# Optimization experiments

Hardware: AMD Instinct MI355X
Metric: run time of the kernel (lower is better)

The kernel has to match this reference:

```python
import jax, jax.numpy as jnp
import numpy as np

U_NUM, I_NUM, ENV_NUM, FACTOR, NNZ, BATCH = 200000, 100000, 4, 64, 9600000, 16384
N_NODES = U_NUM + I_NUM
N_LAYERS = 2


def setup_inputs() -> dict:
    key = jax.random.key(0)
    ks = jax.random.split(key, 14)
    std = 0.01
    user_inv = jax.random.normal(ks[0], (U_NUM, FACTOR), jnp.float32) * std
    item_inv = jax.random.normal(ks[1], (I_NUM, FACTOR), jnp.float32) * std
    user_env = jax.random.normal(ks[2], (U_NUM, FACTOR), jnp.float32) * std
    item_env = jax.random.normal(ks[3], (I_NUM, FACTOR), jnp.float32) * std
    env_emb = jax.random.normal(ks[4], (ENV_NUM, FACTOR), jnp.float32) * std
    # xavier_uniform for classifier weight [env_num, factor]
    limit = float(np.sqrt(6.0 / (FACTOR + ENV_NUM)))
    clf_W = jax.random.uniform(ks[5], (ENV_NUM, FACTOR), jnp.float32, -limit, limit)
    clf_b = jnp.zeros((ENV_NUM,), jnp.float32)
    rows = jax.random.randint(ks[6], (NNZ,), 0, N_NODES, jnp.int32)
    cols = jax.random.randint(ks[7], (NNZ,), 0, N_NODES, jnp.int32)
    # mimic symmetric-normalized adjacency values ~ 1/deg
    vals = jax.random.uniform(ks[8], (NNZ,), jnp.float32) * (1.0 / 32.0)
    users_id = jax.random.randint(ks[9], (BATCH,), 0, U_NUM, jnp.int64)
    items_id = jax.random.randint(ks[10], (BATCH,), 0, I_NUM, jnp.int64)
    envs_id = jax.random.randint(ks[11], (BATCH,), 0, ENV_NUM, jnp.int64)
    return dict(users_id=users_id, items_id=items_id, envs_id=envs_id,
                alpha=jnp.float32(1.0), rows=rows, cols=cols, vals=vals,
                user_inv=user_inv, item_inv=item_inv, user_env=user_env,
                item_env=item_env, env_emb=env_emb, clf_W=clf_W, clf_b=clf_b)


def _lgn_propagate(u_emb, i_emb, rows, cols, vals):
    # LightGCN: mean of [e, Ae, A^2 e]; SpMM via gather + segment_sum
    cur = jnp.concatenate([u_emb, i_emb], axis=0)  # [N, F]
    acc = cur
    for _ in range(N_LAYERS):
        cur = jax.ops.segment_sum(vals[:, None] * cur[cols], rows,
                                  num_segments=N_NODES)
        acc = acc + cur
    light = acc / float(N_LAYERS + 1)
    return light[:U_NUM], light[U_NUM:]


def reference(users_id, items_id, envs_id, alpha, rows, cols, vals,
              user_inv, item_inv, user_env, item_env, env_emb, clf_W, clf_b):
    u_inv_all, i_inv_all = _lgn_propagate(user_inv, item_inv, rows, cols, vals)
    u_env_all, i_env_all = _lgn_propagate(user_env, item_env, rows, cols, vals)
    ue_inv = u_inv_all[users_id]      # [B, F]
    ie_inv = i_inv_all[items_id]
    ue_env = u_env_all[users_id]
    ie_env = i_env_all[items_id]
    e_emb = env_emb[envs_id]
    inv_pref = ue_inv * ie_inv                       # [B, F]
    env_pref = ue_env * ie_env * e_emb               # [B, F]
    invariant_score = jax.nn.sigmoid(jnp.sum(inv_pref, axis=1))
    env_mid = jax.nn.sigmoid(jnp.sum(env_pref, axis=1))
    env_aware_score = invariant_score * env_mid
    # ReverseLayerF is identity in forward
    logits = inv_pref @ clf_W.T + clf_b              # [B, E]
    env_outputs = jax.nn.log_softmax(logits, axis=1)
    return (invariant_score.reshape(-1), env_aware_score.reshape(-1),
            env_outputs.reshape(-1, ENV_NUM))
```

## Files before the change

kernel.cpp:

```cpp
#include <hip/hip_runtime.h>
#include <hip/hip_bf16.h>

#define FACTOR   64
#define F2       128
#define EMAX     8

#define CRPB     512
#define SH1      9
#define MAXNB1   1024
#define CH       16384
#define HCH      32768
#define CAP      18176

#define QSCALE     256.0f
#define INV_QSCALE 0.00390625f

typedef __hip_bfloat162 bf162;
typedef float        f32x2 __attribute__((ext_vector_type(2)));
typedef unsigned int u32x2 __attribute__((ext_vector_type(2)));
typedef unsigned int u32x4 __attribute__((ext_vector_type(4)));

#if __has_builtin(__builtin_amdgcn_cvt_pk_f32_fp8) && __has_builtin(__builtin_amdgcn_cvt_pk_fp8_f32)
#define HAVE_HW_FP8 1
#endif

__device__ __forceinline__ float fp8_dec_sw(unsigned b) {
    unsigned s = (b & 0x80u) << 24;
    unsigned e = (b >> 3) & 0xF;
    unsigned m = b & 7u;
    if (e == 0) {
        float r = (float)m * 0.001953125f;
        return (b & 0x80u) ? -r : r;
    }
    return __uint_as_float(s | ((e + 120u) << 23) | (m << 20));
}

__device__ __forceinline__ unsigned fp8_enc_sw(float f) {
    unsigned x = __float_as_uint(f);
    unsigned s = (x >> 24) & 0x80u;
    float a = fabsf(f);
    if (a < 0.0009765625f) return s;
    if (a >= 448.f) return s | 0x7Eu;
    int e = (int)((__float_as_uint(a) >> 23)) - 127;
    if (e < -6) {
        int m = (int)(a * 512.f + 0.5f);
        if (m >= 8) return s | 0x08u;
        return s | (unsigned)m;
    }
    unsigned mant = (__float_as_uint(a) >> 20) & 0x7u;
    unsigned rnd  = (__float_as_uint(a) >> 19) & 0x1u;
    unsigned code = ((unsigned)(e + 7) << 3) | mant;
    code += rnd;
    if (code >= 0x7Fu) code = 0x7Eu;
    return s | code;
}

__device__ __forceinline__ float2 fp8x2_lo(unsigned u) {
#ifdef HAVE_HW_FP8
    f32x2 r = __builtin_amdgcn_cvt_pk_f32_fp8((int)u, false);
    float2 o; o.x = r.x; o.y = r.y; return o;
#else
    float2 o; o.x = fp8_dec_sw(u & 0xFFu); o.y = fp8_dec_sw((u >> 8) & 0xFFu); return o;
#endif
}
__device__ __forceinline__ float2 fp8x2_hi(unsigned u) {
#ifdef HAVE_HW_FP8
    f32x2 r = __builtin_amdgcn_cvt_pk_f32_fp8((int)u, true);
    float2 o; o.x = r.x; o.y = r.y; return o;
#else
    float2 o; o.x = fp8_dec_sw((u >> 16) & 0xFFu); o.y = fp8_dec_sw((u >> 24) & 0xFFu); return o;
#endif
}

__device__ __forceinline__ unsigned short f32x2_to_fp8(float a, float b) {
#ifdef HAVE_HW_FP8
    int r = __builtin_amdgcn_cvt_pk_fp8_f32(a, b, 0, false);
    return (unsigned short)(r & 0xFFFF);
#else
    return (unsigned short)(fp8_enc_sw(a) | (fp8_enc_sw(b) << 8));
#endif
}

struct alignas(8) EdgeT { int c; float v; };

__device__ __forceinline__ float wsum(float x) {
#pragma unroll
    for (int o = 32; o > 0; o >>= 1) x += __shfl_xor(x, o, 64);
    return x;
}

__global__ void init_ptr_kernel(int* __restrict__ p, int M) {
    int t = blockIdx.x * blockDim.x + threadIdx.x;
    if (t < M) p[t] = 0;
}

__global__ void bucket_hist_kernel(const int* __restrict__ rows, int* __restrict__ bcnt,
                                   long nnz, int NB1) {
    __shared__ int lc[MAXNB1];
    for (int i = threadIdx.x; i < NB1; i += blockDim.x) lc[i] = 0;
    __syncthreads();
    long base = (long)blockIdx.x * HCH;
    long end  = base + HCH; if (end > nnz) end = nnz;
    if (end - base == HCH) {
        const u32x4* rp = (const u32x4*)(rows + base);
        for (int i = threadIdx.x; i < HCH / 4; i += blockDim.x) {
            u32x4 r4 = __builtin_nontemporal_load(rp + i);
            atomicAdd(&lc[r4.x >> SH1], 1);
            atomicAdd(&lc[r4.y >> SH1], 1);
            atomicAdd(&lc[r4.z >> SH1], 1);
            atomicAdd(&lc[r4.w >> SH1], 1);
        }
    } else {
        for (long e = base + threadIdx.x; e < end; e += blockDim.x)
            atomicAdd(&lc[((unsigned)rows[e]) >> SH1], 1);
    }
    __syncthreads();
    for (int i = threadIdx.x; i < NB1; i += blockDim.x)
        if (lc[i]) atomicAdd(&bcnt[i], lc[i]);
}

__global__ void bucket_scan_kernel(const int* __restrict__ bcnt, int* __restrict__ boff,
                                   int* __restrict__ cursor, int NB1) {
    __shared__ int wsums[4];
    int tid = threadIdx.x;
    int lane = tid & 63, wv = tid >> 6;
    int carry = 0;
    for (int base = 0; base < NB1; base += 1024) {
        int idx = base + tid * 4;
        int v0 = (idx + 0 < NB1) ? bcnt[idx + 0] : 0;
        int v1 = (idx + 1 < NB1) ? bcnt[idx + 1] : 0;
        int v2 = (idx + 2 < NB1) ? bcnt[idx + 2] : 0;
        int v3 = (idx + 3 < NB1) ? bcnt[idx + 3] : 0;
        int s1 = v0 + v1 + v2 + v3;
        int s = s1;
#pragma unroll
        for (int o = 1; o < 64; o <<= 1) { int t = __shfl_up(s, o, 64); if (lane >= o) s += t; }
        if (lane == 63) wsums[wv] = s;
        __syncthreads();
        int woff = 0, total = 0;
#pragma unroll
        for (int i = 0; i < 4; i++) { int t = wsums[i]; if (i < wv) woff += t; total += t; }
        int run = carry + woff + (s - s1);
        if (idx + 0 < NB1) { boff[idx + 0] = run; cursor[idx + 0] = run; } run += v0;
        if (idx + 1 < NB1) { boff[idx + 1] = run; cursor[idx + 1] = run; } run += v1;
        if (idx + 2 < NB1) { boff[idx + 2] = run; cursor[idx + 2] = run; } run += v2;
        if (idx + 3 < NB1) { boff[idx + 3] = run; cursor[idx + 3] = run; } run += v3;
        carry += total;
        __syncthreads();
    }
    if (tid == 0) boff[NB1] = carry;
}

__global__ void partition_kernel(const int* __restrict__ rows, const int* __restrict__ cols,
                                 const float* __restrict__ vals, int* __restrict__ cursor,
                                 EdgeT* __restrict__ staged, long nnz, int NB1) {
    extern __shared__ EdgeT ebuf[];
    __shared__ int lc[MAXNB1];
    __shared__ int lof[MAXNB1];
    __shared__ int lb[MAXNB1];
    __shared__ int wsums[16];
    int tid = threadIdx.x;
    long base = (long)blockIdx.x * CH;
    long end  = base + CH; if (end > nnz) end = nnz;
    int m = (int)(end - base);
    for (int i = tid; i < NB1; i += blockDim.x) lc[i] = 0;
    __syncthreads();
    if (m == CH) {
        const u32x4* rp = (const u32x4*)(rows + base);
        for (int i = tid; i < CH / 4; i += blockDim.x) {
            u32x4 r4 = rp[i];
            atomicAdd(&lc[r4.x >> SH1], 1);
            atomicAdd(&lc[r4.y >> SH1], 1);
            atomicAdd(&lc[r4.z >> SH1], 1);
            atomicAdd(&lc[r4.w >> SH1], 1);
        }
    } else {
        for (int i = tid; i < m; i += blockDim.x)
            atomicAdd(&lc[((unsigned)rows[base + i]) >> SH1], 1);
    }
    __syncthreads();
    int v = (tid < NB1) ? lc[tid] : 0;
    int s = v;
#pragma unroll
    for (int o = 1; o < 64; o <<= 1) { int t = __shfl_up(s, o, 64); if ((tid & 63) >= o) s += t; }
    if ((tid & 63) == 63) wsums[tid >> 6] = s;
    __syncthreads();
    int woff = 0;
#pragma unroll
    for (int i = 0; i < 16; i++) if (i < (tid >> 6)) woff += wsums[i];
    if (tid < NB1) {
        lof[tid] = woff + s - v;
        lb[tid]  = v ? atomicAdd(&cursor[tid], v) : 0;
        lc[tid]  = 0;
    }
    __syncthreads();
    for (int i = tid; i < m; i += blockDim.x) {
        int r = rows[base + i];
        unsigned b = ((unsigned)r) >> SH1;
        int rank = atomicAdd(&lc[b], 1);
        EdgeT E;
        E.c = (int)((((unsigned)r & (CRPB - 1)) << 19) |
                    (unsigned)__builtin_nontemporal_load(cols + base + i));
        E.v = __builtin_nontemporal_load(vals + base + i);
        ebuf[lof[b] + rank] = E;
    }
    __syncthreads();
    int wv = tid >> 6, lane = tid & 63, nwv = blockDim.x >> 6;
    for (int b = wv; b < NB1; b += nwv) {
        int c  = lc[b];
        int lo = lof[b];
        int gb = lb[b];
        for (int j = lane; j < c; j += 64)
            staged[(long)gb + j] = ebuf[lo + j];
    }
}

__global__ void coarse_sort_kernel(const int* __restrict__ boff, const EdgeT* __restrict__ staged,
                                   EdgeT* __restrict__ edges, int* __restrict__ p,
                                   int NB1, int N) {
    extern __shared__ EdgeT le[];
    __shared__ int cnt[CRPB];
    __shared__ int rs[CRPB];
    __shared__ int wsum8[CRPB / 64];
    int b = blockIdx.x;
    int start = boff[b], end = boff[b + 1];
    int m = end - start;
    int tid = threadIdx.x;
    if (tid < CRPB) cnt[tid] = 0;
    __syncthreads();
    for (int i = tid; i < m; i += blockDim.x)
        atomicAdd(&cnt[((unsigned)staged[start + i].c) >> 19], 1);
    __syncthreads();
    int v = (tid < CRPB) ? cnt[tid] : 0;
    int s = v;
#pragma unroll
    for (int o = 1; o < 64; o <<= 1) { int t = __shfl_up(s, o, 64); if ((tid & 63) >= o) s += t; }
    if (tid < CRPB && (tid & 63) == 63) wsum8[tid >> 6] = s;
    __syncthreads();
    if (tid < CRPB) {
        int woff = 0;
        int w = tid >> 6;
#pragma unroll
        for (int i = 0; i < CRPB / 64; i++) if (i < w) woff += wsum8[i];
        int ex = woff + s - v;
        rs[tid] = ex;
        int idx = b * CRPB + tid;
        if (idx <= N) p[idx] = start + ex;
        cnt[tid] = 0;
    }
    if (b == NB1 - 1 && tid == 0) p[N] = end;
    __syncthreads();
    bool fits = (m <= CAP);
    for (int i = tid; i < m; i += blockDim.x) {
        EdgeT E = staged[start + i];
        unsigned key = (unsigned)E.c;
        int rl = key >> 19;
        int rank = atomicAdd(&cnt[rl], 1);
        int pos = rs[rl] + rank;
        EdgeT O; O.c = (int)(key & 0x7FFFFu); O.v = E.v;
        if (fits) le[pos] = O;
        else edges[start + pos] = O;
    }
    __syncthreads();
    if (fits) {
        for (int i = tid; i < m; i += blockDim.x)
            edges[start + i] = le[i];
    }
}

__global__ void pack_x0q_kernel(const float* __restrict__ ui, const float* __restrict__ ii,
                                const float* __restrict__ ue, const float* __restrict__ ie,
                                unsigned short* __restrict__ x0q, int N, int U) {
    long t = (long)blockIdx.x * blockDim.x + threadIdx.x;
    if (t >= (long)N * 64) return;
    int node = (int)(t >> 6);
    int q = (int)(t & 63);
    const float* src;
    if (node < U) src = (q < 32) ? ui + (size_t)node * 64 : ue + (size_t)node * 64;
    else          src = (q < 32) ? ii + (size_t)(node - U) * 64 : ie + (size_t)(node - U) * 64;
    f32x2 x = __builtin_nontemporal_load((const f32x2*)src + (q & 31));
    x0q[t] = f32x2_to_fp8(x.x * QSCALE, x.y * QSCALE);
}

__global__ void spmm1_fp8_kernel(const int* __restrict__ p, const EdgeT* __restrict__ edges,
                                 const unsigned char* __restrict__ x0q,
                                 unsigned int* __restrict__ cur1w, long N) {
    long wid = (long)(blockIdx.x * blockDim.x + threadIdx.x) >> 6;
    int lane = threadIdx.x & 63;
    long rA = wid * 2;
    if (rA >= N) return;
    int half = lane >> 5;
    int sub  = lane & 31;
    long r = rA + half;
    int start = 0, end = 0;
    if (r < N) { start = p[r]; end = p[r + 1]; }
    int cnt = end - start;
    int cntA = __shfl(cnt, 0, 64);
    int cntB = __shfl(cnt, 32, 64);
    int mx = cntA > cntB ? cntA : cntB;
    unsigned lo4 = (unsigned)sub * 4u;
    float a0 = 0.f, a1 = 0.f, a2 = 0.f, a3 = 0.f;
    for (int eb = 0; eb < mx; eb += 32) {
        unsigned off = 0; float v = 0.f;
        int idx = start + eb + sub;
        if (idx < end) {
            u32x2 E = __builtin_nontemporal_load((const u32x2*)edges + idx);
            off = E.x << 7;
            v = __uint_as_float(E.y);
        }
        int rem = mx - eb; if (rem > 32) rem = 32;
        int j = 0;
        for (; j + 4 <= rem; j += 4) {
            unsigned o[4]; float w[4];
#pragma unroll
            for (int k = 0; k < 4; k++) {
                o[k] = (unsigned)__shfl((int)off, j + k, 32) + lo4;
                w[k] = __shfl(v, j + k, 32);
            }
            unsigned d[4];
#pragma unroll
            for (int k = 0; k < 4; k++)
                d[k] = *(const unsigned*)(x0q + o[k]);
#pragma unroll
            for (int k = 0; k < 4; k++) {
                float2 f01 = fp8x2_lo(d[k]);
                float2 f23 = fp8x2_hi(d[k]);
                a0 += f01.x * w[k]; a1 += f01.y * w[k];
                a2 += f23.x * w[k]; a3 += f23.y * w[k];
            }
        }
        for (; j < rem; j++) {
            unsigned o0 = (unsigned)__shfl((int)off, j, 32) + lo4;
            float w0 = __shfl(v, j, 32);
            unsigned d0 = *(const unsigned*)(x0q + o0);
            float2 f01 = fp8x2_lo(d0);
            float2 f23 = fp8x2_hi(d0);
            a0 += f01.x * w0; a1 += f01.y * w0;
            a2 += f23.x * w0; a3 += f23.y * w0;
        }
    }
    if (r < N) {
        bf162 h0, h1;
        h0.x = __float2bfloat16(a0 * INV_QSCALE);
        h0.y = __float2bfloat16(a1 * INV_QSCALE);
        h1.x = __float2bfloat16(a2 * INV_QSCALE);
        h1.y = __float2bfloat16(a3 * INV_QSCALE);
        u32x2 st;
        st.x = *(unsigned*)&h0;
        st.y = *(unsigned*)&h1;
        *((u32x2*)(cur1w + (size_t)r * 64) + sub) = st;
    }
}

__global__ void spmm1_csr_kernel(const int* __restrict__ p, const EdgeT* __restrict__ edges,
                                 const float* __restrict__ ui, const float* __restrict__ ii,
                                 const float* __restrict__ ue, const float* __restrict__ ie,
                                 bf162* __restrict__ cur1h, int N, int U) {
    long wid = (long)(blockIdx.x * blockDim.x + threadIdx.x) >> 6;
    int lane = threadIdx.x & 63;
    if (wid >= N) return;
    int r = (int)wid;
    int start = p[r];
    int end   = p[r + 1];
    bool envHalf = lane >= 32;
    int  fi = lane & 31;
    float2 acc = {0.f, 0.f};
    for (int eb = start; eb < end; eb += 64) {
        int rem = end - eb; if (rem > 64) rem = 64;
        int c = 0; float v = 0.f;
        if (lane < rem) { EdgeT E = edges[eb + lane]; c = E.c; v = E.v; }
        for (int j = 0; j < rem; j++) {
            int   cj = __shfl(c, j, 64);
            float vj = __shfl(v, j, 64);
            const float* binv = (cj < U) ? ui + (size_t)cj * 64 : ii + (size_t)(cj - U) * 64;
            const float* benv = (cj < U) ? ue + (size_t)cj * 64 : ie + (size_t)(cj - U) * 64;
            const float2* srow = (const float2*)(envHalf ? benv : binv);
            float2 x = srow[fi];
            acc.x += x.x * vj;
            acc.y += x.y * vj;
        }
    }
    bf162 h;
    h.x = __float2bfloat16(acc.x);
    h.y = __float2bfloat16(acc.y);
    cur1h[(size_t)r * 64 + lane] = h;
}

__global__ void spmm2_csr_kernel(const int* __restrict__ p, const EdgeT* __restrict__ edges,
                                 const int* __restrict__ users, const int* __restrict__ items,
                                 const bf162* __restrict__ cur1h, float2* __restrict__ curC,
                                 int B, int U) {
    long wid = (long)(blockIdx.x * blockDim.x + threadIdx.x) >> 6;
    int lane = threadIdx.x & 63;
    if (wid >= 2 * B) return;
    int node = (wid < B) ? users[wid] : U + items[wid - B];
    int start = p[node];
    int end   = p[node + 1];
    const char* xb = (const char*)cur1h;
    unsigned lo4 = (unsigned)lane * 4u;
    float2 acc = {0.f, 0.f};
    for (int eb = start; eb < end; eb += 64) {
        int rem = end - eb; if (rem > 64) rem = 64;
        unsigned off = 0; float v = 0.f;
        if (lane < rem) {
            u32x2 E = __builtin_nontemporal_load((const u32x2*)(edges + eb) + lane);
            off = E.x << 8;
            v = __uint_as_float(E.y);
        }
        int j = 0;
        for (; j + 8 <= rem; j += 8) {
            unsigned o[8]; float w[8];
#pragma unroll
            for (int k = 0; k < 8; k++) {
                o[k] = (unsigned)__shfl((int)off, j + k, 64) + lo4;
                w[k] = __shfl(v, j + k, 64);
            }
            bf162 a[8];
#pragma unroll
            for (int k = 0; k < 8; k++)
                a[k] = *(const bf162*)(xb + o[k]);
#pragma unroll
            for (int k = 0; k < 8; k++) {
                acc.x += __bfloat162float(a[k].x) * w[k];
                acc.y += __bfloat162float(a[k].y) * w[k];
            }
        }
        for (; j < rem; j++) {
            unsigned o0 = (unsigned)__shfl((int)off, j, 64) + lo4;
            float w0 = __shfl(v, j, 64);
            bf162 a0 = *(const bf162*)(xb + o0);
            acc.x += __bfloat162float(a0.x) * w0;
            acc.y += __bfloat162float(a0.y) * w0;
        }
    }
    curC[(size_t)wid * 64 + lane] = acc;
}

__global__ void out_kernel(const int* __restrict__ users, const int* __restrict__ items,
                           const int* __restrict__ envs,
                           const float* __restrict__ ui, const float* __restrict__ ii,
                           const float* __restrict__ ue, const float* __restrict__ ie,
                           const __hip_bfloat16* __restrict__ cur1h, const float* __restrict__ curC,
                           const float* __restrict__ env_emb, const float* __restrict__ clfW,
                           const float* __restrict__ clfb, float* __restrict__ out,
                           int B, int U, int E) {
    long wid = (long)(blockIdx.x * blockDim.x + threadIdx.x) >> 6;
    int lane = threadIdx.x & 63;
    if (wid >= B) return;
    int u   = users[wid];
    int itm = items[wid];
    int nit = U + itm;
    int ev  = envs[wid];
    size_t ub = (size_t)u * F2, ib = (size_t)nit * F2;
    size_t sub = (size_t)wid * F2, sib = (size_t)(B + wid) * F2;
    const float third = 1.f / 3.f;
    float ue_inv = (ui[(size_t)u * 64 + lane]   + __bfloat162float(cur1h[ub + lane])      + curC[sub + lane])      * third;
    float ue_env = (ue[(size_t)u * 64 + lane]   + __bfloat162float(cur1h[ub + 64 + lane]) + curC[sub + 64 + lane]) * third;
    float ie_inv = (ii[(size_t)itm * 64 + lane] + __bfloat162float(cur1h[ib + lane])      + curC[sib + lane])      * third;
    float ie_env = (ie[(size_t)itm * 64 + lane] + __bfloat162float(cur1h[ib + 64 + lane]) + curC[sib + 64 + lane]) * third;
    float eev  = env_emb[(size_t)ev * 64 + lane];
    float invp = ue_inv * ie_inv;
    float envp = ue_env * ie_env * eev;
    float s_inv = wsum(invp);
    float s_env = wsum(envp);
    float lg[EMAX];
    for (int e2 = 0; e2 < E; e2++)
        lg[e2] = wsum(invp * clfW[(size_t)e2 * 64 + lane]);
    if (lane == 0) {
        float inv_s = 1.f / (1.f + __expf(-s_inv));
        float env_m = 1.f / (1.f + __expf(-s_env));
        out[wid]     = inv_s;
        out[B + wid] = inv_s * env_m;
        float m = -1e30f;
        for (int e2 = 0; e2 < E; e2++) { lg[e2] += clfb[e2]; m = fmaxf(m, lg[e2]); }
        float se = 0.f;
        for (int e2 = 0; e2 < E; e2++) se += __expf(lg[e2] - m);
        float lse = m + __logf(se);
        float* eo = out + (size_t)2 * B + (size_t)wid * E;
        for (int e2 = 0; e2 < E; e2++) eo[e2] = lg[e2] - lse;
    }
}

extern "C" void kernel_launch(void* const* d_in, const int* in_sizes, int n_in,
                              void* d_out, int out_size, void* d_ws, size_t ws_size,
                              hipStream_t stream) {
    const int*   users    = (const int*)d_in[0];
    const int*   items    = (const int*)d_in[1];
    const int*   envs     = (const int*)d_in[2];
    const int*   rows     = (const int*)d_in[4];
    const int*   cols     = (const int*)d_in[5];
    const float* vals     = (const float*)d_in[6];
    const float* user_inv = (const float*)d_in[7];
    const float* item_inv = (const float*)d_in[8];
    const float* user_env = (const float*)d_in[9];
    const float* item_env = (const float*)d_in[10];
    const float* env_emb  = (const float*)d_in[11];
    const float* clf_W    = (const float*)d_in[12];
    const float* clf_b    = (const float*)d_in[13];

    const int  B   = in_sizes[0];
    const long nnz = in_sizes[4];
    const int  U   = in_sizes[7] / FACTOR;
    const int  I   = in_sizes[8] / FACTOR;
    const int  E   = in_sizes[13] > EMAX ? EMAX : in_sizes[13];
    const int  N   = U + I;
    const int  NB1 = (N + CRPB - 1) / CRPB;

    char* ws = (char*)d_ws;
    size_t edgesSz = (size_t)nnz * sizeof(EdgeT);
    size_t reg2Sz  = (size_t)N * 256;
    if (edgesSz > reg2Sz) reg2Sz = edgesSz;
    size_t x0qSz   = (size_t)N * 128;
    size_t curCSz  = (size_t)2 * B * 512;
    size_t auxSz   = (size_t)(3 * MAXNB1 + 2) * 4;
    if (auxSz > curCSz) curCSz = auxSz;
    size_t pSz     = (size_t)(N + 1) * 4;

    size_t need_big = edgesSz + reg2Sz + x0qSz + curCSz + pSz;
    bool   big      = (ws_size >= need_big);

    EdgeT* edges  = (EdgeT*)ws;
    char*  r2     = ws + edgesSz;
    EdgeT* staged = (EdgeT*)r2;
    bf162* cur1h  = (bf162*)r2;
    char*  r3     = r2 + reg2Sz;
    unsigned short* x0q = (unsigned short*)r3;
    char*  r4     = big ? (r3 + x0qSz) : r3;
    float* curC   = (float*)r4;
    int*   p      = (int*)(r4 + curCSz);
    int*   bcnt   = (int*)curC;
    int*   boff   = bcnt + MAXNB1;
    int*   cursor = boff + MAXNB1 + 1;

    const int nHistBlocks = (int)((nnz + HCH - 1) / HCH);
    const int nPartBlocks = (int)((nnz + CH - 1) / CH);
    init_ptr_kernel<<<(NB1 + 255) / 256, 256, 0, stream>>>(bcnt, NB1);
    bucket_hist_kernel<<<nHistBlocks, 1024, 0, stream>>>(rows, bcnt, nnz, NB1);
    bucket_scan_kernel<<<1, 256, 0, stream>>>(bcnt, boff, cursor, NB1);
    partition_kernel<<<nPartBlocks, 1024, (size_t)CH * sizeof(EdgeT), stream>>>(
        rows, cols, vals, cursor, staged, nnz, NB1);
    coarse_sort_kernel<<<NB1, 1024, (size_t)CAP * sizeof(EdgeT), stream>>>(
        boff, staged, edges, p, NB1, N);

    if (big) {
        pack_x0q_kernel<<<(int)(((long)N * 64 + 255) / 256), 256, 0, stream>>>(
            user_inv, item_inv, user_env, item_env, x0q, N, U);
        long nPairs = ((long)N + 1) / 2;
        spmm1_fp8_kernel<<<(int)((nPairs * 64 + 255) / 256), 256, 0, stream>>>(
            p, edges, (const unsigned char*)x0q, (unsigned int*)cur1h, (long)N);
    } else {
        spmm1_csr_kernel<<<(int)(((long)N * 64 + 255) / 256), 256, 0, stream>>>(
            p, edges, user_inv, item_inv, user_env, item_env, cur1h, N, U);
    }

    spmm2_csr_kernel<<<(int)(((long)2 * B * 64 + 255) / 256), 256, 0, stream>>>(
        p, edges, users, items, cur1h, (float2*)curC, B, U);

    out_kernel<<<(int)(((long)B * 64 + 255) / 256), 256, 0, stream>>>(
        users, items, envs, user_inv, item_inv, user_env, item_env,
        (const __hip_bfloat16*)cur1h, curC, env_emb, clf_W, clf_b, (float*)d_out, B, U, E);
}
```

Before: 629.1 us.

## Replace row-per-wave fp8 SpMM with edge-balanced block accumulation in LDS

The first-layer SpMM no longer assigns a half-wave per row. Each block owns 256 rows, its waves split that block's edge range evenly, and partial sums go into a 128 KB fp32 LDS accumulator through shared atomics whenever the row changes. The local row index is kept in the high bits of the edge column word, so the downstream kernels now mask the column. This targets load imbalance and the wasted lanes from per-row edge loops, at the cost of LDS atomics, low occupancy from the large shared allocation, and per-lane scalar edge loads that are replicated across the wave.

```diff
diff --git a/kernel.cpp b/kernel.cpp
--- a/kernel.cpp
+++ b/kernel.cpp
@@ -11,6 +11,7 @@
 #define CH       16384
 #define HCH      32768
 #define CAP      18176
+#define ARPB     256
 
 #define QSCALE     256.0f
 #define INV_QSCALE 0.00390625f
@@ -61,14 +62,6 @@
     float2 o; o.x = r.x; o.y = r.y; return o;
 #else
     float2 o; o.x = fp8_dec_sw(u & 0xFFu); o.y = fp8_dec_sw((u >> 8) & 0xFFu); return o;
-#endif
-}
-__device__ __forceinline__ float2 fp8x2_hi(unsigned u) {
-#ifdef HAVE_HW_FP8
-    f32x2 r = __builtin_amdgcn_cvt_pk_f32_fp8((int)u, true);
-    float2 o; o.x = r.x; o.y = r.y; return o;
-#else
-    float2 o; o.x = fp8_dec_sw((u >> 16) & 0xFFu); o.y = fp8_dec_sw((u >> 24) & 0xFFu); return o;
 #endif
 }
 
@@ -257,9 +250,8 @@
         int rl = key >> 19;
         int rank = atomicAdd(&cnt[rl], 1);
         int pos = rs[rl] + rank;
-        EdgeT O; O.c = (int)(key & 0x7FFFFu); O.v = E.v;
-        if (fits) le[pos] = O;
-        else edges[start + pos] = O;
+        if (fits) le[pos] = E;
+        else edges[start + pos] = E;
     }
     __syncthreads();
     if (fits) {
@@ -282,73 +274,61 @@
     x0q[t] = f32x2_to_fp8(x.x * QSCALE, x.y * QSCALE);
 }
 
-__global__ void spmm1_fp8_kernel(const int* __restrict__ p, const EdgeT* __restrict__ edges,
+__global__ void spmm1_acc_kernel(const int* __restrict__ p, const EdgeT* __restrict__ edges,
                                  const unsigned char* __restrict__ x0q,
-                                 unsigned int* __restrict__ cur1w, long N) {
-    long wid = (long)(blockIdx.x * blockDim.x + threadIdx.x) >> 6;
-    int lane = threadIdx.x & 63;
-    long rA = wid * 2;
-    if (rA >= N) return;
-    int half = lane >> 5;
-    int sub  = lane & 31;
-    long r = rA + half;
-    int start = 0, end = 0;
-    if (r < N) { start = p[r]; end = p[r + 1]; }
-    int cnt = end - start;
-    int cntA = __shfl(cnt, 0, 64);
-    int cntB = __shfl(cnt, 32, 64);
-    int mx = cntA > cntB ? cntA : cntB;
-    unsigned lo4 = (unsigned)sub * 4u;
-    float a0 = 0.f, a1 = 0.f, a2 = 0.f, a3 = 0.f;
-    for (int eb = 0; eb < mx; eb += 32) {
-        unsigned off = 0; float v = 0.f;
-        int idx = start + eb + sub;
-        if (idx < end) {
-            u32x2 E = __builtin_nontemporal_load((const u32x2*)edges + idx);
-            off = E.x << 7;
-            v = __uint_as_float(E.y);
-        }
-        int rem = mx - eb; if (rem > 32) rem = 32;
-        int j = 0;
-        for (; j + 4 <= rem; j += 4) {
-            unsigned o[4]; float w[4];
-#pragma unroll
-            for (int k = 0; k < 4; k++) {
-                o[k] = (unsigned)__shfl((int)off, j + k, 32) + lo4;
-                w[k] = __shfl(v, j + k, 32);
+                                 unsigned int* __restrict__ cur1w, int N) {
+    extern __shared__ float lacc[];
+    int row0 = blockIdx.x * ARPB;
+    int rows = N - row0; if (rows > ARPB) rows = ARPB;
+    int tid = threadIdx.x;
+    for (int i = tid; i < ARPB * 128; i += blockDim.x) lacc[i] = 0.f;
+    __syncthreads();
+    int bs = p[row0], be = p[row0 + rows];
+    int lane = tid & 63, w = tid >> 6, nw = blockDim.x >> 6;
+    long len = be - bs;
+    int cs = bs + (int)(len * w / nw);
+    int ce = bs + (int)(len * (w + 1) / nw);
+    unsigned lo2 = (unsigned)lane * 2u;
+    float a0 = 0.f, a1 = 0.f;
+    int cur = -1;
+    for (int e8 = cs; e8 < ce; e8 += 8) {
+        int n = ce - e8; if (n > 8) n = 8;
+        int   ks[8]; float vs[8]; unsigned short ds[8];
+#pragma unroll
+        for (int k = 0; k < 8; k++) if (k < n) {
+            EdgeT E = edges[e8 + k];
+            ks[k] = E.c; vs[k] = E.v;
+        }
+#pragma unroll
+        for (int k = 0; k < 8; k++) if (k < n)
+            ds[k] = *(const unsigned short*)(
+                x0q + (((size_t)((unsigned)ks[k] & 0x7FFFFu)) << 7) + lo2);
+#pragma unroll
+        for (int k = 0; k < 8; k++) if (k < n) {
+            int rl = (int)(((unsigned)ks[k] >> 19) & (ARPB - 1));
+            if (rl != cur) {
+                if (cur >= 0) {
+                    atomicAdd(&lacc[cur * 128 + (int)lo2], a0);
+                    atomicAdd(&lacc[cur * 128 + (int)lo2 + 1], a1);
+                }
+                cur = rl; a0 = 0.f; a1 = 0.f;
             }
-            unsigned d[4];
-#pragma unroll
-            for (int k = 0; k < 4; k++)
-                d[k] = *(const unsigned*)(x0q + o[k]);
-#pragma unroll
-            for (int k = 0; k < 4; k++) {
-                float2 f01 = fp8x2_lo(d[k]);
-                float2 f23 = fp8x2_hi(d[k]);
-                a0 += f01.x * w[k]; a1 += f01.y * w[k];
-                a2 += f23.x * w[k]; a3 += f23.y * w[k];
-            }
-        }
-        for (; j < rem; j++) {
-            unsigned o0 = (unsigned)__shfl((int)off, j, 32) + lo4;
-            float w0 = __shfl(v, j, 32);
-            unsigned d0 = *(const unsigned*)(x0q + o0);
-            float2 f01 = fp8x2_lo(d0);
-            float2 f23 = fp8x2_hi(d0);
-            a0 += f01.x * w0; a1 += f01.y * w0;
-            a2 += f23.x * w0; a3 += f23.y * w0;
-        }
-    }
-    if (r < N) {
-        bf162 h0, h1;
-        h0.x = __float2bfloat16(a0 * INV_QSCALE);
-        h0.y = __float2bfloat16(a1 * INV_QSCALE);
-        h1.x = __float2bfloat16(a2 * INV_QSCALE);
-        h1.y = __float2bfloat16(a3 * INV_QSCALE);
-        u32x2 st;
-        st.x = *(unsigned*)&h0;
-        st.y = *(unsigned*)&h1;
-        *((u32x2*)(cur1w + (size_t)r * 64) + sub) = st;
+            float2 f = fp8x2_lo((unsigned)ds[k]);
+            a0 += f.x * vs[k];
+            a1 += f.y * vs[k];
+        }
+    }
+    if (cur >= 0) {
+        atomicAdd(&lacc[cur * 128 + (int)lo2], a0);
+        atomicAdd(&lacc[cur * 128 + (int)lo2 + 1], a1);
+    }
+    __syncthreads();
+    for (int i = tid; i < rows * 64; i += blockDim.x) {
+        int r = i >> 6, q = i & 63;
+        bf162 h;
+        h.x = __float2bfloat16(lacc[r * 128 + 2 * q]     * INV_QSCALE);
+        h.y = __float2bfloat16(lacc[r * 128 + 2 * q + 1] * INV_QSCALE);
+        cur1w[(size_t)(row0 + r) * 64 + q] = *(unsigned*)&h;
     }
 }
 
@@ -368,7 +348,7 @@
     for (int eb = start; eb < end; eb += 64) {
         int rem = end - eb; if (rem > 64) rem = 64;
         int c = 0; float v = 0.f;
-        if (lane < rem) { EdgeT E = edges[eb + lane]; c = E.c; v = E.v; }
+        if (lane < rem) { EdgeT E = edges[eb + lane]; c = (int)((unsigned)E.c & 0x7FFFFu); v = E.v; }
         for (int j = 0; j < rem; j++) {
             int   cj = __shfl(c, j, 64);
             float vj = __shfl(v, j, 64);
@@ -404,7 +384,7 @@
         unsigned off = 0; float v = 0.f;
         if (lane < rem) {
             u32x2 E = __builtin_nontemporal_load((const u32x2*)(edges + eb) + lane);
-            off = E.x << 8;
+            off = (E.x & 0x7FFFFu) << 8;
             v = __uint_as_float(E.y);
         }
         int j = 0;
@@ -545,9 +525,9 @@
     if (big) {
         pack_x0q_kernel<<<(int)(((long)N * 64 + 255) / 256), 256, 0, stream>>>(
             user_inv, item_inv, user_env, item_env, x0q, N, U);
-        long nPairs = ((long)N + 1) / 2;
-        spmm1_fp8_kernel<<<(int)((nPairs * 64 + 255) / 256), 256, 0, stream>>>(
-            p, edges, (const unsigned char*)x0q, (unsigned int*)cur1h, (long)N);
+        const int nAccBlocks = (N + ARPB - 1) / ARPB;
+        spmm1_acc_kernel<<<nAccBlocks, 1024, (size_t)ARPB * 128 * 4, stream>>>(
+            p, edges, (const unsigned char*)x0q, (unsigned int*)cur1h, N);
     } else {
         spmm1_csr_kernel<<<(int)(((long)N * 64 + 255) / 256), 256, 0, stream>>>(
             p, edges, user_inv, item_inv, user_env, item_env, cur1h, N, U);
```

After: 2.010 ms. +219.5%, slower.
